# Performance work log

Hardware: AMD Instinct MI355X
Metric: run time of the kernel (lower is better)

Reference implementation:

```python
import jax, jax.numpy as jnp
import numpy as np


def setup_inputs() -> dict:
    key = jax.random.key(0)
    ks = jax.random.split(key, 6)
    B, C, H, W = 8, 1024, 48, 48
    K = 32            # keep_topk
    Cg = C // K       # channels per group = 32
    return {
        "corr_features": jax.random.normal(ks[0], (B, H, W, H, W), jnp.float32),
        "cur_features": jax.random.normal(ks[1], (B, C, H, W), jnp.float32),
        "ref_mask": jax.random.uniform(ks[2], (B, 1, 384, 384), dtype=jnp.float32),
        # grouped 1x1 conv: per-group weight [K, out_per_group, in_per_group]
        "group_w": jax.random.normal(ks[3], (K, Cg, Cg), jnp.float32) * 0.02,
        "group_b": jnp.zeros((C,), jnp.float32),
        # global 1x1 conv: [out=Cg, in=C]
        "global_w": jax.random.normal(ks[4], (Cg, C), jnp.float32) * 0.02,
        "global_b": jnp.zeros((Cg,), jnp.float32),
    }


def reference(corr_features, cur_features, ref_mask, group_w, group_b, global_w, global_b):
    B, ch, cw, rh, rw = corr_features.shape
    C = cur_features.shape[1]
    K, Cg, _ = group_w.shape  # K = keep_topk, Cg = C // K

    cur_flat = cur_features.reshape(B, C, ch * cw)          # [B,C,N]
    corr = corr_features.reshape(B, ch * cw, rh * rw)       # [B,N,M]

    # F.interpolate(..., mode='bilinear', align_corners=False) == half-pixel linear resize
    mask = jax.image.resize(ref_mask, (B, 1, rh, rw), method="linear")
    mask = (mask.reshape(B, 1, rh * rw) > 0.5).astype(jnp.float32)
    fg_corr = corr * mask                                    # [B,N,M]

    # get_struct_info: topk over summed correlation, gather channel features
    scores = fg_corr.sum(axis=-1)                            # [B,N]
    _, idx = jax.lax.top_k(scores, K)                        # [B,K]
    struct = jnp.take_along_axis(cur_flat, idx[:, None, :], axis=2)  # [B,C,K]
    struct = jnp.swapaxes(struct, 1, 2)                      # [B,K,C]

    # bmm(struct, cur_flat): [B,K,C] x [B,C,N] -> [B,K,N]
    struct_info = jnp.einsum('bkc,bcn->bkn', struct, cur_flat).reshape(B, K, ch, cw)

    # grouped 1x1 conv (groups=K) + ReLU
    xg = cur_features.reshape(B, K, Cg, ch, cw)
    group_feat = jnp.einsum('bkihw,koi->bkohw', xg, group_w)
    group_feat = jax.nn.relu(group_feat + group_b.reshape(K, Cg)[None, :, :, None, None])

    # repeat struct_info across each group's Cg channels, multiply, sum over groups
    group_struct = (struct_info[:, :, None, :, :] * group_feat).sum(axis=1)  # [B,Cg,H,W]

    # global 1x1 conv + ReLU
    global_feat = jnp.einsum('bchw,oc->bohw', cur_features, global_w)
    global_feat = jax.nn.relu(global_feat + global_b[None, :, None, None])   # [B,Cg,H,W]
    global_struct = struct_info.mean(axis=1, keepdims=True) * global_feat

    return jnp.concatenate([group_struct, global_struct], axis=1)  # [B,2*Cg,H,W]
```

## Files before the change

### kernel.cpp

```cpp
#include <hip/hip_runtime.h>
#include <math.h>

#define BB 8
#define CC 1024
#define HW 48
#define NN 2304
#define MM 2304
#define KK 32

typedef __attribute__((ext_vector_type(8))) short short8v;
typedef __attribute__((ext_vector_type(4))) float f32x4;

__device__ __forceinline__ unsigned short f2bf(float f) {
    unsigned u = __float_as_uint(f);
    return (unsigned short)((u + 0x7FFFu + ((u >> 16) & 1u)) >> 16);
}

__global__ void mask_kernel(const float* __restrict__ rm, float* __restrict__ mask) {
    int t = blockIdx.x * 256 + threadIdx.x;
    if (t >= BB * NN) return;
    int b = t / NN, p = t % NN;
    int y = p / HW, x = p % HW;
    const float* src = rm + (size_t)b * 384 * 384;

    int jx0 = 8 * x - 4;
    float wx[16];
    float wxs = 0.f;
    #pragma unroll
    for (int dx = 0; dx < 16; ++dx) {
        int jx = jx0 + dx;
        float w = 1.0f - fabsf((float)dx - 7.5f) * 0.125f;
        if (jx >= 0 && jx < 384) { wx[dx] = w; wxs += w; } else wx[dx] = 0.f;
    }
    int jy0 = 8 * y - 4;
    float acc = 0.f, wys = 0.f;
    for (int dy = 0; dy < 16; ++dy) {
        int jy = jy0 + dy;
        if (jy < 0 || jy >= 384) continue;
        float wy = 1.0f - fabsf((float)dy - 7.5f) * 0.125f;
        wys += wy;
        const float* row = src + (size_t)jy * 384;
        float rs = 0.f;
        #pragma unroll
        for (int dx = 0; dx < 16; ++dx) {
            if (wx[dx] > 0.f) rs += wx[dx] * row[jx0 + dx];
        }
        acc += wy * rs;
    }
    float v = acc / (wys * wxs);
    mask[t] = (v > 0.5f) ? 1.0f : 0.0f;
}

__global__ void scores_kernel(const float* __restrict__ corr, const float* __restrict__ mask,
                              float* __restrict__ scores) {
    int wave = threadIdx.x >> 6, lane = threadIdx.x & 63;
    int row = blockIdx.x * 4 + wave;
    int b = row / NN, n = row % NN;
    const float4* cr = (const float4*)(corr + ((size_t)b * NN + n) * MM);
    const float4* mr = (const float4*)(mask + (size_t)b * MM);
    float acc = 0.f;
    #pragma unroll
    for (int it = 0; it < 9; ++it) {
        int i = it * 64 + lane;
        float4 cv = cr[i];
        float4 mv = mr[i];
        acc += cv.x * mv.x + cv.y * mv.y + cv.z * mv.z + cv.w * mv.w;
    }
    #pragma unroll
    for (int off = 32; off >= 1; off >>= 1) acc += __shfl_down(acc, off);
    if (lane == 0) scores[row] = acc;
}

__global__ void topk1_kernel(const float* __restrict__ scores,
                             float* __restrict__ cval, int* __restrict__ cidx) {
    int b = blockIdx.x >> 3, ch = blockIdx.x & 7;
    int t = threadIdx.x;
    const float* s = scores + b * NN + ch * 288;
    float v0 = s[t];
    float v1 = (t < 32) ? s[256 + t] : -INFINITY;
    int i0 = t, i1 = 256 + t;
    __shared__ float wv[4]; __shared__ int wi[4];
    __shared__ int bwi;
    for (int it = 0; it < KK; ++it) {
        float bv = (v0 >= v1) ? v0 : v1;
        int   bi = (v0 >= v1) ? i0 : i1;
        #pragma unroll
        for (int off = 32; off >= 1; off >>= 1) {
            float ov = __shfl_down(bv, off);
            int   oi = __shfl_down(bi, off);
            if (ov > bv || (ov == bv && oi < bi)) { bv = ov; bi = oi; }
        }
        if ((t & 63) == 0) { wv[t >> 6] = bv; wi[t >> 6] = bi; }
        __syncthreads();
        if (t == 0) {
            #pragma unroll
            for (int u = 1; u < 4; ++u)
                if (wv[u] > bv || (wv[u] == bv && wi[u] < bi)) { bv = wv[u]; bi = wi[u]; }
            bwi = bi;
            cval[(b * 8 + ch) * 32 + it] = bv;
            cidx[(b * 8 + ch) * 32 + it] = ch * 288 + bi;
        }
        __syncthreads();
        int W = bwi;
        if (i0 == W) v0 = -INFINITY;
        if (i1 == W) v1 = -INFINITY;
    }
}

__global__ void topk2_kernel(const float* __restrict__ cval, const int* __restrict__ cidx,
                             int* __restrict__ idxo) {
    int b = blockIdx.x, t = threadIdx.x;
    float v = cval[b * 256 + t];
    int gi = cidx[b * 256 + t];
    __shared__ float wv[4]; __shared__ int wi[4];
    __shared__ int bwi_s;
    for (int it = 0; it < KK; ++it) {
        float bv = v; int bi = gi;
        #pragma unroll
        for (int off = 32; off >= 1; off >>= 1) {
            float ov = __shfl_down(bv, off);
            int   oi = __shfl_down(bi, off);
            if (ov > bv || (ov == bv && oi < bi)) { bv = ov; bi = oi; }
        }
        if ((t & 63) == 0) { wv[t >> 6] = bv; wi[t >> 6] = bi; }
        __syncthreads();
        if (t == 0) {
            #pragma unroll
            for (int u = 1; u < 4; ++u)
                if (wv[u] > bv || (wv[u] == bv && wi[u] < bi)) { bv = wv[u]; bi = wi[u]; }
            idxo[b * KK + it] = bi;
            bwi_s = bi;
        }
        __syncthreads();
        if (gi == bwi_s) v = -INFINITY;
    }
}

__global__ void gather_kernel(const float* __restrict__ cur, const int* __restrict__ idx,
                              unsigned short* __restrict__ st) {
    int t = blockIdx.x * 256 + threadIdx.x;
    int c = t & (CC - 1); int bk = t >> 10; int k = bk & 31; int b = bk >> 5;
    int id = idx[b * KK + k];
    st[t] = f2bf(cur[((size_t)b * CC + c) * NN + id]);
}

__global__ void wconv_kernel(const float* __restrict__ gw, const float* __restrict__ glw,
                             unsigned short* __restrict__ gwh, unsigned short* __restrict__ glwh) {
    int t = blockIdx.x * 256 + threadIdx.x;
    gwh[t] = f2bf(gw[t]);
    glwh[t] = f2bf(glw[t]);
}

__global__ __launch_bounds__(256) void fused_mfma(
    const float* __restrict__ cur, const unsigned short* __restrict__ st16,
    const unsigned short* __restrict__ gwh, const unsigned short* __restrict__ glwh,
    const float* __restrict__ gb, const float* __restrict__ glb,
    float* __restrict__ out)
{
    __shared__ unsigned short XT[16 * 1024];
    __shared__ float SIL[32][18];
    __shared__ float PART[4][2][256];
    __shared__ float MS[16];
    __shared__ float GBL[CC];
    __shared__ float GLBL[32];

    int hw = blockIdx.x;
    int b = hw & 7;
    int n0 = (hw >> 3) * 16;
    int t = threadIdx.x;
    int w = t >> 6, l = t & 63;
    int mrow = w & 1, mat = w >> 1;
    int nrow = l & 15, kq = l >> 4;

    for (int i = t; i < CC; i += 256) GBL[i] = gb[i];
    if (t < 32) GLBL[t] = glb[t];

    const float* curb = cur + (size_t)b * CC * NN;
    int nq = t & 3, ci0 = t >> 2;
    #pragma unroll
    for (int q = 0; q < 8; ++q) {
        int ci = ci0 + 64 * q;
        int c = 2 * ci;
        const float* p0 = curb + (size_t)c * NN + n0 + 4 * nq;
        float4 f0 = *(const float4*)p0;
        float4 f1 = *(const float4*)(p0 + NN);
        float a0[4] = {f0.x, f0.y, f0.z, f0.w};
        float a1[4] = {f1.x, f1.y, f1.z, f1.w};
        #pragma unroll
        for (int r = 0; r < 4; ++r) {
            int n = 4 * nq + r;
            unsigned pk = (unsigned)f2bf(a0[r]) | ((unsigned)f2bf(a1[r]) << 16);
            *(unsigned*)((char*)XT + n * 2048 + ((((ci >> 2) ^ (n & 7)) << 4) + ((ci & 3) << 2))) = pk;
        }
    }
    __syncthreads();

    const char* xbase = (const char*)XT + nrow * 2048;
    const unsigned short* Abase = (mat == 0 ? st16 + (size_t)b * KK * CC : glwh)
                                  + (size_t)(16 * mrow + nrow) * CC + 8 * kq;
    f32x4 acc = {0.f, 0.f, 0.f, 0.f};
    #pragma unroll 8
    for (int cc = 0; cc < 32; ++cc) {
        short8v A = *(const short8v*)(Abase + cc * 32);
        short8v B = *(const short8v*)(xbase + (((cc * 4 + kq) ^ (nrow & 7)) << 4));
        acc = __builtin_amdgcn_mfma_f32_16x16x32_bf16(A, B, acc, 0, 0, 0);
    }

    if (mat == 0) {
        #pragma unroll
        for (int r = 0; r < 4; ++r)
            SIL[16 * mrow + 4 * kq + r][nrow] = acc[r];
    }
    __syncthreads();
    if (t < 16) {
        float s = 0.f;
        #pragma unroll
        for (int k = 0; k < 32; ++k) s += SIL[k][t];
        MS[t] = s * (1.0f / 32.0f);
    }

    f32x4 p0 = {0.f, 0.f, 0.f, 0.f}, p1 = {0.f, 0.f, 0.f, 0.f};
    const f32x4 zz = {0.f, 0.f, 0.f, 0.f};
    #pragma unroll
    for (int j = 0; j < 8; ++j) {
        int k = 8 * w + j;
        const unsigned short* gk = gwh + k * 1024 + 8 * kq;
        short8v A0 = *(const short8v*)(gk + nrow * 32);
        short8v A1 = *(const short8v*)(gk + (16 + nrow) * 32);
        short8v B = *(const short8v*)(xbase + (((k * 4 + kq) ^ (nrow & 7)) << 4));
        f32x4 g0 = __builtin_amdgcn_mfma_f32_16x16x32_bf16(A0, B, zz, 0, 0, 0);
        f32x4 g1 = __builtin_amdgcn_mfma_f32_16x16x32_bf16(A1, B, zz, 0, 0, 0);
        float sik = SIL[k][nrow];
        #pragma unroll
        for (int r = 0; r < 4; ++r) {
            p0[r] += sik * fmaxf(g0[r] + GBL[k * 32 + 4 * kq + r], 0.f);
            p1[r] += sik * fmaxf(g1[r] + GBL[k * 32 + 16 + 4 * kq + r], 0.f);
        }
    }
    *(f32x4*)&PART[w][0][l * 4] = p0;
    *(f32x4*)&PART[w][1][l * 4] = p1;
    __syncthreads();

    size_t ob = (size_t)b * 64 * NN + n0 + nrow;
    if (mat == 0) {
        #pragma unroll
        for (int r = 0; r < 4; ++r) {
            int li = l * 4 + r;
            float v = PART[0][mrow][li] + PART[1][mrow][li]
                    + PART[2][mrow][li] + PART[3][mrow][li];
            out[ob + (size_t)(16 * mrow + 4 * kq + r) * NN] = v;
        }
    } else {
        float msv = MS[nrow];
        #pragma unroll
        for (int r = 0; r < 4; ++r) {
            int o = 16 * mrow + 4 * kq + r;
            out[ob + (size_t)(32 + o) * NN] = fmaxf(acc[r] + GLBL[o], 0.f) * msv;
        }
    }
}

extern "C" void kernel_launch(void* const* d_in, const int* in_sizes, int n_in,
                              void* d_out, int out_size, void* d_ws, size_t ws_size,
                              hipStream_t stream) {
    const float* corr = (const float*)d_in[0];
    const float* cur  = (const float*)d_in[1];
    const float* rm   = (const float*)d_in[2];
    const float* gw   = (const float*)d_in[3];
    const float* gb   = (const float*)d_in[4];
    const float* glw  = (const float*)d_in[5];
    const float* glb  = (const float*)d_in[6];
    float* out = (float*)d_out;
    float* ws  = (float*)d_ws;

    float* mask   = ws;
    float* scores = mask + BB * MM;
    float* cval   = scores + BB * NN;
    int*   cidx   = (int*)(cval + 2048);
    int*   idx    = cidx + 2048;
    unsigned short* st16 = (unsigned short*)(idx + 256);
    unsigned short* gwh  = st16 + BB * KK * CC;
    unsigned short* glwh = gwh + 32768;

    mask_kernel<<<(BB * NN + 255) / 256, 256, 0, stream>>>(rm, mask);
    scores_kernel<<<BB * NN / 4, 256, 0, stream>>>(corr, mask, scores);
    topk1_kernel<<<BB * 8, 256, 0, stream>>>(scores, cval, cidx);
    topk2_kernel<<<BB, 256, 0, stream>>>(cval, cidx, idx);
    gather_kernel<<<BB * KK * CC / 256, 256, 0, stream>>>(cur, idx, st16);
    wconv_kernel<<<128, 256, 0, stream>>>(gw, glw, gwh, glwh);
    fused_mfma<<<BB * (NN / 16), 256, 0, stream>>>(cur, st16, gwh, glwh, gb, glb, out);
}
```

Measured before the change: 165.0 us.

## Fuse two-stage top-k, gather and weight conversion into one kernel

Replaces the two-pass top-k, the gather kernel and the weight bf16 conversion with a single launch. Eight blocks each run a single-pass top-32 over one batch's 2304 scores, then gather the selected columns. The remaining blocks convert weights. Separately, the MFMA kernel now aliases the PART buffer onto the XT shared buffer, with an extra barrier, to reduce LDS use and possibly raise occupancy. The cost is less parallelism in the top-k and gather, since only 8 blocks do that serial work.

```diff
diff --git a/kernel.cpp b/kernel.cpp
--- a/kernel.cpp
+++ b/kernel.cpp
@@ -71,84 +71,66 @@
     if (lane == 0) scores[row] = acc;
 }
 
-__global__ void topk1_kernel(const float* __restrict__ scores,
-                             float* __restrict__ cval, int* __restrict__ cidx) {
-    int b = blockIdx.x >> 3, ch = blockIdx.x & 7;
-    int t = threadIdx.x;
-    const float* s = scores + b * NN + ch * 288;
-    float v0 = s[t];
-    float v1 = (t < 32) ? s[256 + t] : -INFINITY;
-    int i0 = t, i1 = 256 + t;
-    __shared__ float wv[4]; __shared__ int wi[4];
-    __shared__ int bwi;
+__global__ __launch_bounds__(512) void topk_gather_wconv(
+    const float* __restrict__ scores, const float* __restrict__ cur,
+    const float* __restrict__ gw, const float* __restrict__ glw,
+    unsigned short* __restrict__ st, unsigned short* __restrict__ gwh,
+    unsigned short* __restrict__ glwh)
+{
+    int blk = blockIdx.x, t = threadIdx.x;
+    if (blk >= 8) {
+        int e = (blk - 8) * 512 + t;
+        gwh[e] = f2bf(gw[e]);
+        gwh[e + 16384] = f2bf(gw[e + 16384]);
+        glwh[e] = f2bf(glw[e]);
+        glwh[e + 16384] = f2bf(glw[e + 16384]);
+        return;
+    }
+    int b = blk;
+    float v[5];
+    #pragma unroll
+    for (int j = 0; j < 5; ++j) {
+        int e = t + 512 * j;
+        v[j] = (e < NN) ? scores[b * NN + e] : -INFINITY;
+    }
+    __shared__ float wv[8]; __shared__ int wi[8];
+    __shared__ int idxL[KK];
+    __shared__ int bcast;
+    int lane = t & 63, w = t >> 6;
     for (int it = 0; it < KK; ++it) {
-        float bv = (v0 >= v1) ? v0 : v1;
-        int   bi = (v0 >= v1) ? i0 : i1;
+        float bv = -INFINITY; int bi = 1 << 30;
+        #pragma unroll
+        for (int j = 0; j < 5; ++j) {
+            int e = t + 512 * j;
+            if (v[j] > bv) { bv = v[j]; bi = e; }
+        }
         #pragma unroll
         for (int off = 32; off >= 1; off >>= 1) {
             float ov = __shfl_down(bv, off);
             int   oi = __shfl_down(bi, off);
             if (ov > bv || (ov == bv && oi < bi)) { bv = ov; bi = oi; }
         }
-        if ((t & 63) == 0) { wv[t >> 6] = bv; wi[t >> 6] = bi; }
+        if (lane == 0) { wv[w] = bv; wi[w] = bi; }
         __syncthreads();
         if (t == 0) {
             #pragma unroll
-            for (int u = 1; u < 4; ++u)
+            for (int u = 1; u < 8; ++u)
                 if (wv[u] > bv || (wv[u] == bv && wi[u] < bi)) { bv = wv[u]; bi = wi[u]; }
-            bwi = bi;
-            cval[(b * 8 + ch) * 32 + it] = bv;
-            cidx[(b * 8 + ch) * 32 + it] = ch * 288 + bi;
+            idxL[it] = bi;
+            bcast = bi;
         }
         __syncthreads();
-        int W = bwi;
-        if (i0 == W) v0 = -INFINITY;
-        if (i1 == W) v1 = -INFINITY;
-    }
-}
-
-__global__ void topk2_kernel(const float* __restrict__ cval, const int* __restrict__ cidx,
-                             int* __restrict__ idxo) {
-    int b = blockIdx.x, t = threadIdx.x;
-    float v = cval[b * 256 + t];
-    int gi = cidx[b * 256 + t];
-    __shared__ float wv[4]; __shared__ int wi[4];
-    __shared__ int bwi_s;
-    for (int it = 0; it < KK; ++it) {
-        float bv = v; int bi = gi;
-        #pragma unroll
-        for (int off = 32; off >= 1; off >>= 1) {
-            float ov = __shfl_down(bv, off);
-            int   oi = __shfl_down(bi, off);
-            if (ov > bv || (ov == bv && oi < bi)) { bv = ov; bi = oi; }
-        }
-        if ((t & 63) == 0) { wv[t >> 6] = bv; wi[t >> 6] = bi; }
-        __syncthreads();
-        if (t == 0) {
-            #pragma unroll
-            for (int u = 1; u < 4; ++u)
-                if (wv[u] > bv || (wv[u] == bv && wi[u] < bi)) { bv = wv[u]; bi = wi[u]; }
-            idxo[b * KK + it] = bi;
-            bwi_s = bi;
-        }
-        __syncthreads();
-        if (gi == bwi_s) v = -INFINITY;
-    }
-}
-
-__global__ void gather_kernel(const float* __restrict__ cur, const int* __restrict__ idx,
-                              unsigned short* __restrict__ st) {
-    int t = blockIdx.x * 256 + threadIdx.x;
-    int c = t & (CC - 1); int bk = t >> 10; int k = bk & 31; int b = bk >> 5;
-    int id = idx[b * KK + k];
-    st[t] = f2bf(cur[((size_t)b * CC + c) * NN + id]);
-}
-
-__global__ void wconv_kernel(const float* __restrict__ gw, const float* __restrict__ glw,
-                             unsigned short* __restrict__ gwh, unsigned short* __restrict__ glwh) {
-    int t = blockIdx.x * 256 + threadIdx.x;
-    gwh[t] = f2bf(gw[t]);
-    glwh[t] = f2bf(glw[t]);
+        int W = bcast;
+        #pragma unroll
+        for (int j = 0; j < 5; ++j)
+            if (t + 512 * j == W) v[j] = -INFINITY;
+    }
+    const float* curb = cur + (size_t)b * CC * NN;
+    unsigned short* stb = st + b * (KK * CC);
+    for (int e = t; e < KK * CC; e += 512) {
+        int k = e >> 10, c = e & (CC - 1);
+        stb[e] = f2bf(curb[(size_t)c * NN + idxL[k]]);
+    }
 }
 
 __global__ __launch_bounds__(256) void fused_mfma(
@@ -157,9 +139,10 @@
     const float* __restrict__ gb, const float* __restrict__ glb,
     float* __restrict__ out)
 {
-    __shared__ unsigned short XT[16 * 1024];
+    __shared__ __align__(16) char SMEM[32768];
+    unsigned short* XT = (unsigned short*)SMEM;
+    float (*PART)[2][256] = (float (*)[2][256])SMEM;
     __shared__ float SIL[32][18];
-    __shared__ float PART[4][2][256];
     __shared__ float MS[16];
     __shared__ float GBL[CC];
     __shared__ float GLBL[32];
@@ -237,6 +220,7 @@
             p1[r] += sik * fmaxf(g1[r] + GBL[k * 32 + 16 + 4 * kq + r], 0.f);
         }
     }
+    __syncthreads();
     *(f32x4*)&PART[w][0][l * 4] = p0;
     *(f32x4*)&PART[w][1][l * 4] = p1;
     __syncthreads();
@@ -275,18 +259,12 @@
 
     float* mask   = ws;
     float* scores = mask + BB * MM;
-    float* cval   = scores + BB * NN;
-    int*   cidx   = (int*)(cval + 2048);
-    int*   idx    = cidx + 2048;
-    unsigned short* st16 = (unsigned short*)(idx + 256);
+    unsigned short* st16 = (unsigned short*)(scores + BB * NN);
     unsigned short* gwh  = st16 + BB * KK * CC;
     unsigned short* glwh = gwh + 32768;
 
     mask_kernel<<<(BB * NN + 255) / 256, 256, 0, stream>>>(rm, mask);
     scores_kernel<<<BB * NN / 4, 256, 0, stream>>>(corr, mask, scores);
-    topk1_kernel<<<BB * 8, 256, 0, stream>>>(scores, cval, cidx);
-    topk2_kernel<<<BB, 256, 0, stream>>>(cval, cidx, idx);
-    gather_kernel<<<BB * KK * CC / 256, 256, 0, stream>>>(cur, idx, st16);
-    wconv_kernel<<<128, 256, 0, stream>>>(gw, glw, gwh, glwh);
+    topk_gather_wconv<<<40, 512, 0, stream>>>(scores, cur, gw, glw, st16, gwh, glwh);
     fused_mfma<<<BB * (NN / 16), 256, 0, stream>>>(cur, st16, gwh, glwh, gb, glb, out);
 }
```

Result: slower. 186.4 us (+13.0%).
